# Kernel tuning notes

Measured on AMD Instinct MI355X. Metric: run time of the kernel, lower is better.

Reference implementation:

```python
import jax, jax.numpy as jnp
import numpy as np

B = 512; S = 6; Q = 2            # meta-batch, n_way*k_shot, n_way*q_query
DIM = 64; IMG = 28; N_WAY = 2
HEADS = 4; HD = DIM // HEADS     # retrieval heads / head dim
EPS = 1e-5


def _pool_mat(inp, out):
    # exact torch AdaptiveAvgPool2d windowing as a matrix [out, inp]
    P = np.zeros((out, inp), np.float32)
    for i in range(out):
        s = (i * inp) // out
        e = -((-(i + 1) * inp) // out)
        P[i, s:e] = 1.0 / (e - s)
    return jnp.asarray(P)

P28 = _pool_mat(IMG, 8)  # 28 -> 8; subsequent 8 -> 8 pools are identity


def _gelu(x):
    return jax.nn.gelu(x, approximate=False)


def _conv(x, w, b):
    y = jax.lax.conv_general_dilated(x, w, (1, 1), ((1, 1), (1, 1)),
                                     dimension_numbers=('NCHW', 'OIHW', 'NCHW'))
    return y + b[None, :, None, None]


def _bn(x, p):
    # p rows: gamma, beta, running_mean, running_var (eval-mode BatchNorm2d)
    g, bt, m, v = p[0], p[1], p[2], p[3]
    sc = g / jnp.sqrt(v + EPS)
    return (x - m[None, :, None, None]) * sc[None, :, None, None] + bt[None, :, None, None]


def _img_in(x, c1w, c1b, bn1, c2w, c2b, bn2, c3w, c3b, bn3, c4w, c4b, bn4, lin_w):
    h = _bn(_conv(x, c1w, c1b), bn1)
    h = jnp.einsum('oi,ncij,pj->ncop', P28, h, P28)   # adaptive avg pool 28x28 -> 8x8
    h = _gelu(h)                                       # dropout is identity in eval
    h = _gelu(_bn(_conv(h, c2w, c2b), bn2))
    h = _gelu(_bn(_conv(h, c3w, c3b), bn3))
    h = _gelu(_bn(_conv(h, c4w, c4b), bn4))            # -> [N,1,8,8]
    h = h.reshape(h.shape[0], -1)                      # [N,64]
    return h @ lin_w.T                                 # Linear(64 -> DIM, no bias)


def _net(x, w1, w2):
    # x: [B,K,D]; w1,w2: [B,D,D] batched fast weights
    h = jnp.einsum('bed,bkd->bke', w1, x)
    ah = _gelu(h)
    y = jnp.einsum('bed,bkd->bke', w2, ah)
    return y, h


def _get_lor(x, w1, w2, r_q, r_k, r_v, r_o, ln_w, ln_b):
    b, k, _ = x.shape
    q, _ = _net(x, w1, w2)
    qh = jnp.einsum('nhd,bkd->bknh', r_q, q)
    sc = jnp.einsum('bknh,rnh->bknr', qh, r_k) / (HD ** 0.5)
    p = jax.nn.softmax(sc, axis=-1)
    lor = jnp.einsum('bknr,rnh->bknh', p, r_v).reshape(b, k, DIM)
    lor = jnp.einsum('de,bkd->bke', r_o, lor)
    z = lor + x
    mu = z.mean(-1, keepdims=True)
    var = ((z - mu) ** 2).mean(-1, keepdims=True)
    return (z - mu) / jnp.sqrt(var + EPS) * ln_w + ln_b


def _forward(query_w, sxs, qxs, inner_lr, c1w, c1b, bn1, c2w, c2b, bn2, c3w, c3b, bn3,
             c4w, c4b, bn4, lin_w, emb, w1, w2, tags, r_q, r_k, r_v, r_o, ln_w, ln_b,
             sys, qys):
    b = query_w.shape[0]
    s = sxs.shape[1]
    q = qxs.shape[1]
    feats = lambda im: _img_in(im.reshape(-1, 1, IMG, IMG), c1w, c1b, bn1, c2w, c2b,
                               bn2, c3w, c3b, bn3, c4w, c4b, bn4, lin_w)
    sx = feats(sxs).reshape(b, s, DIM)
    qx = feats(qxs).reshape(b, q, DIM)
    qe = tags[4]
    w1b = jnp.broadcast_to(w1, (b, DIM, DIM))
    w2b = jnp.broadcast_to(w2, (b, DIM, DIM))
    bound = sx + emb[sys]                                          # [B,S,D]
    # all 4 tag variants for all S shots in one vectorized get_lor call
    inp = (bound[:, :, None, :] + tags[:4][None, None]).reshape(b, s * 4, DIM)
    lors = _get_lor(inp, w1b, w2b, r_q, r_k, r_v, r_o, ln_w, ln_b).reshape(b, s, 4, DIM)
    l1s, r1s, l2s, r2s = lors[:, :, 0], lors[:, :, 1], lors[:, :, 2], lors[:, :, 3]
    qw1 = w1[None] + jnp.einsum('bsl,bsr->blr', l1s, r1s)
    qw2 = w2[None] + jnp.einsum('bsl,bsr->blr', l2s, r2s)
    preds, _ = _net(qx + qe, qw1, qw2)                             # [B,Q,D]
    logits = jnp.einsum('ld,bqd->bql', emb, preds).reshape(-1, N_WAY)
    labels = qys.reshape(-1)
    ls = jax.nn.log_softmax(logits)
    task_loss = -jnp.take_along_axis(ls, labels[:, None], axis=1).mean()
    n_correct = (jnp.argmax(logits, axis=1) == labels).sum()
    return task_loss, n_correct, b * q


def setup_inputs() -> dict:
    key = jax.random.key(0)
    ks = jax.random.split(key, 24)
    rn = lambda i, sh, sc=1.0: sc * jax.random.normal(ks[i], sh, jnp.float32)
    def bnp(i, c):
        k0, k1, k2 = jax.random.split(ks[i], 3)
        return jnp.stack([1.0 + 0.1 * jax.random.normal(k0, (c,)),
                          0.1 * jax.random.normal(k1, (c,)),
                          0.1 * jax.random.normal(k2, (c,)),
                          0.5 + jax.random.uniform(jax.random.fold_in(ks[i], 3), (c,))])
    return {
        'query_w': rn(0, (B, DIM)),
        'sxs': rn(1, (B, S, IMG * IMG)),
        'qxs': rn(2, (B, Q, IMG * IMG)),
        'inner_lr': jnp.float32(0.1),
        'c1w': rn(3, (32, 1, 3, 3), 0.3), 'c1b': rn(4, (32,), 0.1), 'bn1': bnp(5, 32),
        'c2w': rn(6, (32, 32, 3, 3), 0.06), 'c2b': rn(7, (32,), 0.1), 'bn2': bnp(8, 32),
        'c3w': rn(9, (32, 32, 3, 3), 0.06), 'c3b': rn(10, (32,), 0.1), 'bn3': bnp(11, 32),
        'c4w': rn(12, (1, 32, 3, 3), 0.06), 'c4b': rn(13, (1,), 0.1), 'bn4': bnp(14, 1),
        'lin_w': rn(15, (DIM, 64), 0.125),
        'emb': rn(16, (N_WAY, DIM), 0.125),
        'w1': rn(17, (DIM, DIM), 0.125),
        'w2': rn(18, (DIM, DIM), 0.125),
        'tags': rn(19, (8, DIM), 0.125),
        'r_q': rn(20, (HEADS, HD, DIM), 0.125),
        'r_k': rn(21, (16, HEADS, HD), 0.25),
        'r_v': rn(22, (16, HEADS, HD), 0.25),
        'r_o': rn(23, (DIM, DIM), 0.125),
        'ln_w': 0.001 * jnp.ones((DIM,), jnp.float32),
        'ln_b': jnp.zeros((DIM,), jnp.float32),
        'sys': jax.random.randint(jax.random.fold_in(key, 100), (B, S), 0, N_WAY),
        'qys': jax.random.randint(jax.random.fold_in(key, 101), (B, Q), 0, N_WAY),
    }


def reference(query_w, sxs, qxs, inner_lr, c1w, c1b, bn1, c2w, c2b, bn2, c3w, c3b, bn3,
              c4w, c4b, bn4, lin_w, emb, w1, w2, tags, r_q, r_k, r_v, r_o, ln_w, ln_b,
              sys, qys):
    task_loss, n_correct, n_q = _forward(query_w, sxs, qxs, inner_lr, c1w, c1b, bn1,
                                         c2w, c2b, bn2, c3w, c3b, bn3, c4w, c4b, bn4,
                                         lin_w, emb, w1, w2, tags, r_q, r_k, r_v, r_o,
                                         ln_w, ln_b, sys, qys)
    return (task_loss, task_loss, jnp.float32(0.0), n_correct, n_q)
```

## Files before the change

kernel.cpp:

```cpp
#include <hip/hip_runtime.h>
#include <math.h>

constexpr int NSUP = 3072;
constexpr float EPSF = 1e-5f;

constexpr int WS_W1B  = 0;
constexpr int WS_B1   = 1024;
constexpr int WS_W2B  = 1056;
constexpr int WS_W3B  = 5664;
constexpr int WS_W4B  = 10272;
constexpr int WS_B4   = 10416;
constexpr int WS_B2   = 10420;
constexpr int WS_B3   = 10452;
constexpr int WS_HW1  = 10484;
constexpr int WS_HW2  = 12788;
constexpr int WS_HRQ  = 15092;
constexpr int WS_HROT = 17396;
constexpr int WS_PART = 19700;
constexpr int WS_FEATS= 20724;

using short8 = __attribute__((ext_vector_type(8))) short;
using f32x4  = __attribute__((ext_vector_type(4))) float;

__device__ __forceinline__ float gelu_f(float x) {
    return 0.5f * x * (1.0f + erff(x * 0.70710678118654752440f));
}
__device__ __forceinline__ unsigned short f2bf(float f) {
    unsigned u = __float_as_uint(f);
    return (unsigned short)((u + 0x7FFFu + ((u >> 16) & 1u)) >> 16);
}
__device__ __forceinline__ float bflo(unsigned u) { return __uint_as_float(u << 16); }
__device__ __forceinline__ float bfhi(unsigned u) { return __uint_as_float(u & 0xffff0000u); }

__global__ void __launch_bounds__(256) precompute_kernel(
    const float* __restrict__ c1w, const float* __restrict__ c1b, const float* __restrict__ bn1,
    const float* __restrict__ c2w, const float* __restrict__ c2b, const float* __restrict__ bn2,
    const float* __restrict__ c3w, const float* __restrict__ c3b, const float* __restrict__ bn3,
    const float* __restrict__ c4w, const float* __restrict__ c4b, const float* __restrict__ bn4,
    const float* __restrict__ w1, const float* __restrict__ w2,
    const float* __restrict__ rq, const float* __restrict__ ro,
    float* __restrict__ ws)
{
    const int gid = blockIdx.x * 256 + threadIdx.x;
    const int gsz = gridDim.x * 256;

    unsigned short* w1b = (unsigned short*)(ws + WS_W1B);
    for (int v = gid; v < 2048; v += gsz) {
        int kt = v >> 10, rem = v & 1023, oc = rem >> 5, kk = rem & 31;
        int tap = kt * 32 + kk;
        unsigned short o = 0;
        if (tap < 36) {
            int tt = tap / 6, s = tap - tt * 6;
            float sum = 0.f;
            for (int di = 0; di < 3; ++di) {
                int a = tt - di; if (a < 0 || a > 3) continue;
                for (int dj = 0; dj < 3; ++dj) {
                    int bb = s - dj; if (bb < 0 || bb > 3) continue;
                    sum += c1w[oc * 9 + di * 3 + dj];
                }
            }
            float sc1 = bn1[oc] * rsqrtf(bn1[96 + oc] + EPSF);
            o = f2bf(sum * sc1 * (1.0f / 16.0f));
        }
        w1b[v] = o;
    }
    for (int c = gid; c < 32; c += gsz) {
        float sc1 = bn1[c] * rsqrtf(bn1[96 + c] + EPSF);
        ws[WS_B1 + c] = (c1b[c] - bn1[64 + c]) * sc1 + bn1[32 + c];
        float sc2 = bn2[c] * rsqrtf(bn2[96 + c] + EPSF);
        ws[WS_B2 + c] = (c2b[c] - bn2[64 + c]) * sc2 + bn2[32 + c];
        float sc3 = bn3[c] * rsqrtf(bn3[96 + c] + EPSF);
        ws[WS_B3 + c] = (c3b[c] - bn3[64 + c]) * sc3 + bn3[32 + c];
    }
    unsigned short* w2b = (unsigned short*)(ws + WS_W2B);
    unsigned short* w3b = (unsigned short*)(ws + WS_W3B);
    for (int v = gid; v < 9216; v += gsz) {
        int tap = v >> 10, oc = (v >> 5) & 31, ic = v & 31;
        float sc2 = bn2[oc] * rsqrtf(bn2[96 + oc] + EPSF);
        float sc3 = bn3[oc] * rsqrtf(bn3[96 + oc] + EPSF);
        w2b[v] = f2bf(c2w[oc * 288 + ic * 9 + tap] * sc2);
        w3b[v] = f2bf(c3w[oc * 288 + ic * 9 + tap] * sc3);
    }
    {
        unsigned short* w4b = (unsigned short*)(ws + WS_W4B);
        float sc4 = bn4[0] * rsqrtf(bn4[3] + EPSF);
        for (int v = gid; v < 288; v += gsz) {
            int tap = v >> 5, ic = v & 31;
            w4b[v] = f2bf(c4w[ic * 9 + tap] * sc4);
        }
        if (gid == 0) ws[WS_B4] = (c4b[0] - bn4[2]) * sc4 + bn4[1];
    }
    unsigned short* hw1 = (unsigned short*)(ws + WS_HW1);
    unsigned short* hw2 = (unsigned short*)(ws + WS_HW2);
    unsigned short* hrq = (unsigned short*)(ws + WS_HRQ);
    unsigned short* hro = (unsigned short*)(ws + WS_HROT);
    for (int v = gid; v < 4608; v += gsz) {
        int e = v / 72, d = v - e * 72;
        unsigned short a = 0, b = 0, c = 0, r = 0;
        if (d < 64) {
            a = f2bf(w1[e * 64 + d]);
            b = f2bf(w2[e * 64 + d]);
            c = f2bf(rq[e * 64 + d]);
            r = f2bf(ro[d * 64 + e]);
        }
        hw1[v] = a; hw2[v] = b; hrq[v] = c; hro[v] = r;
    }
}

__global__ void __launch_bounds__(256, 4) feats_kernel(
    const float* __restrict__ sxs, const float* __restrict__ qxs,
    const float* __restrict__ lin_w, const float* __restrict__ ws,
    float* __restrict__ feats)
{
    __shared__ __align__(16) unsigned short sAct[4][3200];
    __shared__ __align__(16) float sh4[4][64];

    const int t    = threadIdx.x;
    const int wv   = t >> 6;
    const int lane = t & 63;
    const int col  = lane & 15;
    const int quad = lane >> 4;
    const int n    = blockIdx.x * 4 + wv;

    unsigned short* A = sAct[wv];

    {
        uint4 z = {0, 0, 0, 0};
        for (int i = lane; i < 400; i += 64) ((uint4*)A)[i] = z;
    }

    {
        const unsigned short* w1b = (const unsigned short*)(ws + WS_W1B);
        const float* img = (n < NSUP) ? (sxs + (size_t)n * 784) : (qxs + (size_t)(n - NSUP) * 784);
        int ttj[8], ssj[8];
        #pragma unroll
        for (int j = 0; j < 8; ++j) {
            int k = quad * 8 + j;
            ttj[j] = k / 6; ssj[j] = k - ttj[j] * 6;
        }
        f32x4 acc[4][2];
        #pragma unroll
        for (int mt = 0; mt < 4; ++mt) { acc[mt][0] = (f32x4){0,0,0,0}; acc[mt][1] = (f32x4){0,0,0,0}; }

        short8 b00 = *(const short8*)(w1b + (0 * 16 + col) * 32 + quad * 8);
        short8 b01 = *(const short8*)(w1b + (1 * 16 + col) * 32 + quad * 8);
        short8 b10 = *(const short8*)(w1b + 1024 + (0 * 16 + col) * 32 + quad * 8);
        short8 b11 = *(const short8*)(w1b + 1024 + (1 * 16 + col) * 32 + quad * 8);

        #pragma unroll
        for (int mt = 0; mt < 4; ++mt) {
            int px = mt * 16 + col;
            int sr = (((px >> 3) * 7) >> 1) - 1;
            int sc = (((px & 7) * 7) >> 1) - 1;
            short8 a0;
            #pragma unroll
            for (int j = 0; j < 8; ++j) {
                int rr = sr + ttj[j], cc = sc + ssj[j];
                float v = ((unsigned)rr < 28u && (unsigned)cc < 28u) ? img[rr * 28 + cc] : 0.f;
                a0[j] = (short)f2bf(v);
            }
            acc[mt][0] = __builtin_amdgcn_mfma_f32_16x16x32_bf16(a0, b00, acc[mt][0], 0, 0, 0);
            acc[mt][1] = __builtin_amdgcn_mfma_f32_16x16x32_bf16(a0, b01, acc[mt][1], 0, 0, 0);
            short8 a1 = {0,0,0,0,0,0,0,0};
            if (quad == 0) {
                #pragma unroll
                for (int j = 0; j < 4; ++j) {
                    int rr = sr + 5, cc = sc + 2 + j;
                    float v = ((unsigned)rr < 28u && (unsigned)cc < 28u) ? img[rr * 28 + cc] : 0.f;
                    a1[j] = (short)f2bf(v);
                }
            }
            acc[mt][0] = __builtin_amdgcn_mfma_f32_16x16x32_bf16(a1, b10, acc[mt][0], 0, 0, 0);
            acc[mt][1] = __builtin_amdgcn_mfma_f32_16x16x32_bf16(a1, b11, acc[mt][1], 0, 0, 0);
        }
        float bi0 = ws[WS_B1 + col], bi1 = ws[WS_B1 + 16 + col];
        #pragma unroll
        for (int mt = 0; mt < 4; ++mt)
            #pragma unroll
            for (int reg = 0; reg < 4; ++reg) {
                int px = mt * 16 + quad * 4 + reg;
                unsigned short* dst = A + (((px >> 3) + 1) * 10 + (px & 7) + 1) * 32;
                dst[col]      = f2bf(gelu_f(acc[mt][0][reg] + bi0));
                dst[col + 16] = f2bf(gelu_f(acc[mt][1][reg] + bi1));
            }
    }

    #pragma unroll 1
    for (int layer = 0; layer < 2; ++layer) {
        const unsigned short* wb = (const unsigned short*)(ws + (layer ? WS_W3B : WS_W2B));
        f32x4 acc[4][2];
        #pragma unroll
        for (int mt = 0; mt < 4; ++mt) { acc[mt][0] = (f32x4){0,0,0,0}; acc[mt][1] = (f32x4){0,0,0,0}; }
        const unsigned short* abase[4];
        #pragma unroll
        for (int mt = 0; mt < 4; ++mt) {
            int px = mt * 16 + col;
            abase[mt] = A + ((px >> 3) * 10 + (px & 7)) * 32 + quad * 8;
        }
        #pragma unroll
        for (int dr = 0; dr < 3; ++dr)
            #pragma unroll
            for (int dc = 0; dc < 3; ++dc) {
                int tap = dr * 3 + dc;
                short8 b0 = *(const short8*)(wb + (tap * 32 + col) * 32 + quad * 8);
                short8 b1 = *(const short8*)(wb + (tap * 32 + 16 + col) * 32 + quad * 8);
                #pragma unroll
                for (int mt = 0; mt < 4; ++mt) {
                    short8 a = *(const short8*)(abase[mt] + (dr * 10 + dc) * 32);
                    acc[mt][0] = __builtin_amdgcn_mfma_f32_16x16x32_bf16(a, b0, acc[mt][0], 0, 0, 0);
                    acc[mt][1] = __builtin_amdgcn_mfma_f32_16x16x32_bf16(a, b1, acc[mt][1], 0, 0, 0);
                }
            }
        float bi0 = ws[(layer ? WS_B3 : WS_B2) + col];
        float bi1 = ws[(layer ? WS_B3 : WS_B2) + 16 + col];
        #pragma unroll
        for (int mt = 0; mt < 4; ++mt)
            #pragma unroll
            for (int reg = 0; reg < 4; ++reg) {
                int px = mt * 16 + quad * 4 + reg;
                unsigned short* dst = A + (((px >> 3) + 1) * 10 + (px & 7) + 1) * 32;
                dst[col]      = f2bf(gelu_f(acc[mt][0][reg] + bi0));
                dst[col + 16] = f2bf(gelu_f(acc[mt][1][reg] + bi1));
            }
    }

    {
        f32x4 acc4[4];
        #pragma unroll
        for (int mt = 0; mt < 4; ++mt) acc4[mt] = (f32x4){0,0,0,0};
        const unsigned short* abase[4];
        #pragma unroll
        for (int mt = 0; mt < 4; ++mt) {
            int px = mt * 16 + col;
            abase[mt] = A + ((px >> 3) * 10 + (px & 7)) * 32 + quad * 8;
        }
        const unsigned short* w4g = (const unsigned short*)(ws + WS_W4B);
        #pragma unroll
        for (int dr = 0; dr < 3; ++dr)
            #pragma unroll
            for (int dc = 0; dc < 3; ++dc) {
                int tap = dr * 3 + dc;
                short8 b = *(const short8*)(w4g + tap * 32 + quad * 8);
                #pragma unroll
                for (int mt = 0; mt < 4; ++mt) {
                    short8 a = *(const short8*)(abase[mt] + (dr * 10 + dc) * 32);
                    acc4[mt] = __builtin_amdgcn_mfma_f32_16x16x32_bf16(a, b, acc4[mt], 0, 0, 0);
                }
            }
        if (col < 4) {
            f32x4 v = acc4[0];
            if (col == 1) v = acc4[1];
            else if (col == 2) v = acc4[2];
            else if (col == 3) v = acc4[3];
            float b4 = ws[WS_B4];
            #pragma unroll
            for (int reg = 0; reg < 4; ++reg)
                sh4[wv][col * 16 + quad * 4 + reg] = gelu_f(v[reg] + b4);
        }
    }

    {
        const float4* lw = (const float4*)(lin_w + (size_t)lane * 64);
        const float4* hp = (const float4*)sh4[wv];
        float acc = 0.f;
        #pragma unroll
        for (int j = 0; j < 16; ++j) {
            float4 w = lw[j], h = hp[j];
            acc += w.x * h.x + w.y * h.y + w.z * h.z + w.w * h.w;
        }
        feats[n * 64 + lane] = acc;
    }
}

__device__ __forceinline__ void head_gemm(const unsigned short* __restrict__ Ab,
                                          const unsigned short* __restrict__ Bw,
                                          int col, int quad, int wvid, f32x4 res[2])
{
    #pragma unroll
    for (int u = 0; u < 2; ++u) {
        int tau = wvid + u * 4;
        int mt = tau & 1, nt = tau >> 1;
        f32x4 acc = {0, 0, 0, 0};
        #pragma unroll
        for (int kt = 0; kt < 2; ++kt) {
            short8 a = *(const short8*)(Ab + (mt * 16 + col) * 72 + kt * 32 + quad * 8);
            short8 b = *(const short8*)(Bw + (nt * 16 + col) * 72 + kt * 32 + quad * 8);
            acc = __builtin_amdgcn_mfma_f32_16x16x32_bf16(a, b, acc, 0, 0, 0);
        }
        res[u] = acc;
    }
}

__global__ void __launch_bounds__(256, 4) head_kernel(
    const float* __restrict__ emb, const float* __restrict__ tags,
    const float* __restrict__ rk, const float* __restrict__ rv,
    const float* __restrict__ lnw, const float* __restrict__ lnb,
    const int* __restrict__ sys, const int* __restrict__ qys,
    const float* __restrict__ ws, const float* __restrict__ feats,
    float* __restrict__ part)
{
    __shared__ __align__(16) unsigned short bufA[2304], bufB[2304];
    __shared__ __align__(16) float sXf[1536];
    __shared__ __align__(16) float s_xq[128], s_ah[128], s_yp[128];
    __shared__ float s_t1[12], s_t2[12], s_mu[24], s_rs[24], s_lg[4];

    const int t    = threadIdx.x;
    const int b    = blockIdx.x;
    const int wvid = t >> 6;
    const int col  = t & 15;
    const int quad = (t >> 4) & 3;

    const unsigned short* W1g = (const unsigned short*)(ws + WS_HW1);
    const unsigned short* W2g = (const unsigned short*)(ws + WS_HW2);
    const unsigned short* RQg = (const unsigned short*)(ws + WS_HRQ);
    const unsigned short* ROg = (const unsigned short*)(ws + WS_HROT);

    if (t < 72) {
        uint4 z = {0, 0, 0, 0};
        ((uint4*)(bufA + 1728))[t] = z;
        ((uint4*)(bufB + 1728))[t] = z;
    }
    for (int idx = t; idx < 1536; idx += 256) {
        int k = idx >> 6, e = idx & 63;
        int s = k >> 2, tg = k & 3;
        int cls = sys[b * 6 + s];
        float v = feats[(b * 6 + s) * 64 + e] + emb[cls * 64 + e] + tags[tg * 64 + e];
        sXf[idx] = v;
        bufA[k * 72 + e] = f2bf(v);
    }
    __syncthreads();

    f32x4 r[2];
    head_gemm(bufA, W1g, col, quad, wvid, r);
    #pragma unroll
    for (int u = 0; u < 2; ++u) {
        int tau = wvid + u * 4, mt = tau & 1, nt = tau >> 1;
        #pragma unroll
        for (int reg = 0; reg < 4; ++reg) {
            int row = mt * 16 + quad * 4 + reg;
            if (row < 24) bufB[row * 72 + nt * 16 + col] = f2bf(gelu_f(r[u][reg]));
        }
    }
    __syncthreads();
    head_gemm(bufB, W2g, col, quad, wvid, r);
    #pragma unroll
    for (int u = 0; u < 2; ++u) {
        int tau = wvid + u * 4, mt = tau & 1, nt = tau >> 1;
        #pragma unroll
        for (int reg = 0; reg < 4; ++reg) {
            int row = mt * 16 + quad * 4 + reg;
            if (row < 24) bufA[row * 72 + nt * 16 + col] = f2bf(r[u][reg]);
        }
    }
    __syncthreads();
    head_gemm(bufA, RQg, col, quad, wvid, r);
    #pragma unroll
    for (int u = 0; u < 2; ++u) {
        int tau = wvid + u * 4, mt = tau & 1, nt = tau >> 1;
        #pragma unroll
        for (int reg = 0; reg < 4; ++reg) {
            int row = mt * 16 + quad * 4 + reg;
            if (row < 24) bufB[row * 72 + nt * 16 + col] = f2bf(r[u][reg]);
        }
    }
    __syncthreads();

    if (t < 96) {
        int k = t >> 2, nn = t & 3;
        const unsigned short* qp = bufB + k * 72 + nn * 16;
        uint4 u0 = *(const uint4*)(qp);
        uint4 u1 = *(const uint4*)(qp + 8);
        float qv[16];
        qv[0]=bflo(u0.x); qv[1]=bfhi(u0.x); qv[2]=bflo(u0.y); qv[3]=bfhi(u0.y);
        qv[4]=bflo(u0.z); qv[5]=bfhi(u0.z); qv[6]=bflo(u0.w); qv[7]=bfhi(u0.w);
        qv[8]=bflo(u1.x); qv[9]=bfhi(u1.x); qv[10]=bflo(u1.y); qv[11]=bfhi(u1.y);
        qv[12]=bflo(u1.z); qv[13]=bfhi(u1.z); qv[14]=bflo(u1.w); qv[15]=bfhi(u1.w);
        float sc[16]; float mx = -1e30f;
        #pragma unroll
        for (int rr = 0; rr < 16; ++rr) {
            const float* kp = rk + rr * 64 + nn * 16;
            float d = 0.f;
            #pragma unroll
            for (int h = 0; h < 16; ++h) d += qv[h] * kp[h];
            d *= 0.25f;
            sc[rr] = d; mx = fmaxf(mx, d);
        }
        float sum = 0.f;
        #pragma unroll
        for (int rr = 0; rr < 16; ++rr) { sc[rr] = expf(sc[rr] - mx); sum += sc[rr]; }
        float inv = 1.0f / sum;
        float o[16];
        #pragma unroll
        for (int h = 0; h < 16; ++h) o[h] = 0.f;
        #pragma unroll
        for (int rr = 0; rr < 16; ++rr) {
            const float* vp = rv + rr * 64 + nn * 16;
            float p = sc[rr];
            #pragma unroll
            for (int h = 0; h < 16; ++h) o[h] += p * vp[h];
        }
        unsigned short* op = bufA + k * 72 + nn * 16;
        #pragma unroll
        for (int h = 0; h < 16; ++h) op[h] = f2bf(o[h] * inv);
    }
    __syncthreads();

    head_gemm(bufA, ROg, col, quad, wvid, r);
    #pragma unroll
    for (int u = 0; u < 2; ++u) {
        int tau = wvid + u * 4, mt = tau & 1, nt = tau >> 1;
        #pragma unroll
        for (int reg = 0; reg < 4; ++reg) {
            int row = mt * 16 + quad * 4 + reg;
            if (row < 24) {
                int idx = row * 64 + nt * 16 + col;
                sXf[idx] = sXf[idx] + r[u][reg];
            }
        }
    }
    __syncthreads();

    if (t < 24) {
        const float4* zp = (const float4*)(sXf + t * 64);
        float sx_ = 0.f;
        #pragma unroll
        for (int j = 0; j < 16; ++j) {
            float4 v = zp[(j + t) & 15];
            sx_ += v.x + v.y + v.z + v.w;
        }
        float mu = sx_ * (1.0f / 64.0f);
        float vv = 0.f;
        #pragma unroll
        for (int j = 0; j < 16; ++j) {
            float4 v = zp[(j + t) & 15];
            float d0 = v.x - mu, d1 = v.y - mu, d2 = v.z - mu, d3 = v.w - mu;
            vv += d0*d0 + d1*d1 + d2*d2 + d3*d3;
        }
        s_mu[t] = mu;
        s_rs[t] = 1.0f / sqrtf(vv * (1.0f / 64.0f) + EPSF);
    }
    __syncthreads();
    for (int idx = t; idx < 1536; idx += 256) {
        int k = idx >> 6, e = idx & 63;
        float v = (sXf[idx] - s_mu[k]) * s_rs[k] * lnw[e] + lnb[e];
        bufB[k * 72 + e] = f2bf(v);
    }
    if (t < 128) {
        int q = t >> 6, e = t & 63;
        s_xq[t] = feats[(NSUP + b * 2 + q) * 64 + e] + tags[256 + e];
    }
    __syncthreads();

    if (t < 12) {
        int q = t / 6, s = t - q * 6;
        const uint4* rp = (const uint4*)(bufB + (s * 4 + 1) * 72);
        const float* xp = s_xq + q * 64;
        float d = 0.f;
        #pragma unroll
        for (int j = 0; j < 8; ++j) {
            uint4 u = rp[j];
            const float* x = xp + j * 8;
            d += bflo(u.x)*x[0] + bfhi(u.x)*x[1] + bflo(u.y)*x[2] + bfhi(u.y)*x[3]
               + bflo(u.z)*x[4] + bfhi(u.z)*x[5] + bflo(u.w)*x[6] + bfhi(u.w)*x[7];
        }
        s_t1[t] = d;
    }
    __syncthreads();
    if (t < 128) {
        int q = t >> 6, e = t & 63;
        const uint4* wp = (const uint4*)(W1g + e * 72);
        const float* xp = s_xq + q * 64;
        float acc = 0.f;
        #pragma unroll
        for (int j = 0; j < 8; ++j) {
            uint4 u = wp[j];
            const float* x = xp + j * 8;
            acc += bflo(u.x)*x[0] + bfhi(u.x)*x[1] + bflo(u.y)*x[2] + bfhi(u.y)*x[3]
                 + bflo(u.z)*x[4] + bfhi(u.z)*x[5] + bflo(u.w)*x[6] + bfhi(u.w)*x[7];
        }
        #pragma unroll
        for (int s = 0; s < 6; ++s)
            acc += bflo((unsigned)bufB[(s * 4 + 0) * 72 + e]) * s_t1[q * 6 + s];
        s_ah[t] = gelu_f(acc);
    }
    __syncthreads();
    if (t < 12) {
        int q = t / 6, s = t - q * 6;
        const uint4* rp = (const uint4*)(bufB + (s * 4 + 3) * 72);
        const float* xp = s_ah + q * 64;
        float d = 0.f;
        #pragma unroll
        for (int j = 0; j < 8; ++j) {
            uint4 u = rp[j];
            const float* x = xp + j * 8;
            d += bflo(u.x)*x[0] + bfhi(u.x)*x[1] + bflo(u.y)*x[2] + bfhi(u.y)*x[3]
               + bflo(u.z)*x[4] + bfhi(u.z)*x[5] + bflo(u.w)*x[6] + bfhi(u.w)*x[7];
        }
        s_t2[t] = d;
    }
    __syncthreads();
    if (t < 128) {
        int q = t >> 6, e = t & 63;
        const uint4* wp = (const uint4*)(W2g + e * 72);
        const float* xp = s_ah + q * 64;
        float acc = 0.f;
        #pragma unroll
        for (int j = 0; j < 8; ++j) {
            uint4 u = wp[j];
            const float* x = xp + j * 8;
            acc += bflo(u.x)*x[0] + bfhi(u.x)*x[1] + bflo(u.y)*x[2] + bfhi(u.y)*x[3]
                 + bflo(u.z)*x[4] + bfhi(u.z)*x[5] + bflo(u.w)*x[6] + bfhi(u.w)*x[7];
        }
        #pragma unroll
        for (int s = 0; s < 6; ++s)
            acc += bflo((unsigned)bufB[(s * 4 + 2) * 72 + e]) * s_t2[q * 6 + s];
        s_yp[t] = acc;
    }
    __syncthreads();
    if (t < 4) {
        int q = t >> 1, ll = t & 1;
        const float4* ep = (const float4*)(emb + ll * 64);
        const float4* yp = (const float4*)(s_yp + q * 64);
        float d = 0.f;
        #pragma unroll
        for (int j = 0; j < 16; ++j) {
            float4 a = ep[j], x = yp[j];
            d += a.x*x.x + a.y*x.y + a.z*x.z + a.w*x.w;
        }
        s_lg[t] = d;
    }
    __syncthreads();
    if (t == 0) {
        float lsum = 0.f, corr = 0.f;
        #pragma unroll
        for (int q = 0; q < 2; ++q) {
            float l0 = s_lg[q * 2], l1 = s_lg[q * 2 + 1];
            int lab = qys[b * 2 + q];
            float m = fmaxf(l0, l1);
            float lse = m + logf(expf(l0 - m) + expf(l1 - m));
            lsum += -((lab ? l1 : l0) - lse);
            int pred = (l1 > l0) ? 1 : 0;
            corr += (pred == lab) ? 1.0f : 0.0f;
        }
        part[b] = lsum;
        part[512 + b] = corr;
    }
}

__global__ void __launch_bounds__(256) finalize_kernel(const float* __restrict__ part,
                                                       float* __restrict__ out)
{
    __shared__ float sl[256], sc[256];
    const int t = threadIdx.x;
    sl[t] = part[t] + part[t + 256];
    sc[t] = part[512 + t] + part[768 + t];
    __syncthreads();
    for (int s = 128; s > 0; s >>= 1) {
        if (t < s) { sl[t] += sl[t + s]; sc[t] += sc[t + s]; }
        __syncthreads();
    }
    if (t == 0) {
        float loss = sl[0] * (1.0f / 1024.0f);
        out[0] = loss;
        out[1] = loss;
        out[2] = 0.0f;
        out[3] = sc[0];
        out[4] = 1024.0f;
    }
}

extern "C" void kernel_launch(void* const* d_in, const int* in_sizes, int n_in,
                              void* d_out, int out_size, void* d_ws, size_t ws_size,
                              hipStream_t stream)
{
    (void)in_sizes; (void)n_in; (void)out_size; (void)ws_size;
    const float* sxs  = (const float*)d_in[1];
    const float* qxs  = (const float*)d_in[2];
    const float* c1w  = (const float*)d_in[4];
    const float* c1b  = (const float*)d_in[5];
    const float* bn1  = (const float*)d_in[6];
    const float* c2w  = (const float*)d_in[7];
    const float* c2b  = (const float*)d_in[8];
    const float* bn2  = (const float*)d_in[9];
    const float* c3w  = (const float*)d_in[10];
    const float* c3b  = (const float*)d_in[11];
    const float* bn3  = (const float*)d_in[12];
    const float* c4w  = (const float*)d_in[13];
    const float* c4b  = (const float*)d_in[14];
    const float* bn4  = (const float*)d_in[15];
    const float* lin_w= (const float*)d_in[16];
    const float* emb  = (const float*)d_in[17];
    const float* w1   = (const float*)d_in[18];
    const float* w2   = (const float*)d_in[19];
    const float* tags = (const float*)d_in[20];
    const float* rq   = (const float*)d_in[21];
    const float* rk   = (const float*)d_in[22];
    const float* rv   = (const float*)d_in[23];
    const float* ro   = (const float*)d_in[24];
    const float* lnw  = (const float*)d_in[25];
    const float* lnb  = (const float*)d_in[26];
    const int*   sys  = (const int*)d_in[27];
    const int*   qys  = (const int*)d_in[28];

    float* ws  = (float*)d_ws;
    float* out = (float*)d_out;

    precompute_kernel<<<64, 256, 0, stream>>>(c1w, c1b, bn1, c2w, c2b, bn2,
                                              c3w, c3b, bn3, c4w, c4b, bn4,
                                              w1, w2, rq, ro, ws);
    feats_kernel<<<1024, 256, 0, stream>>>(sxs, qxs, lin_w, ws, ws + WS_FEATS);
    head_kernel<<<512, 256, 0, stream>>>(emb, tags, rk, rv, lnw, lnb, sys, qys,
                                         ws, ws + WS_FEATS, ws + WS_PART);
    finalize_kernel<<<1, 256, 0, stream>>>(ws + WS_PART, out);
}
```

Baseline: 175.7 us.

## Fuse feature extraction and per-task head into one 512-thread kernel

```diff
diff --git a/kernel.cpp b/kernel.cpp
--- a/kernel.cpp
+++ b/kernel.cpp
@@ -1,7 +1,6 @@
 #include <hip/hip_runtime.h>
 #include <math.h>
 
-constexpr int NSUP = 3072;
 constexpr float EPSF = 1e-5f;
 
 constexpr int WS_W1B  = 0;
@@ -17,7 +16,6 @@
 constexpr int WS_HRQ  = 15092;
 constexpr int WS_HROT = 17396;
 constexpr int WS_PART = 19700;
-constexpr int WS_FEATS= 20724;
 
 using short8 = __attribute__((ext_vector_type(8))) short;
 using f32x4  = __attribute__((ext_vector_type(4))) float;
@@ -107,23 +105,51 @@
     }
 }
 
-__global__ void __launch_bounds__(256, 4) feats_kernel(
+__device__ __forceinline__ f32x4 head_gemm8(const unsigned short* __restrict__ Ab,
+                                            const unsigned short* __restrict__ Bw,
+                                            int col, int quad, int tau)
+{
+    int mt = tau & 1, nt = tau >> 1;
+    f32x4 acc = {0, 0, 0, 0};
+    #pragma unroll
+    for (int kt = 0; kt < 2; ++kt) {
+        short8 a = *(const short8*)(Ab + (mt * 16 + col) * 72 + kt * 32 + quad * 8);
+        short8 b = *(const short8*)(Bw + (nt * 16 + col) * 72 + kt * 32 + quad * 8);
+        acc = __builtin_amdgcn_mfma_f32_16x16x32_bf16(a, b, acc, 0, 0, 0);
+    }
+    return acc;
+}
+
+__global__ void __launch_bounds__(512, 2) fused_kernel(
     const float* __restrict__ sxs, const float* __restrict__ qxs,
-    const float* __restrict__ lin_w, const float* __restrict__ ws,
-    float* __restrict__ feats)
+    const float* __restrict__ lin_w,
+    const float* __restrict__ emb, const float* __restrict__ tags,
+    const float* __restrict__ rk, const float* __restrict__ rv,
+    const float* __restrict__ lnw, const float* __restrict__ lnb,
+    const int* __restrict__ sys, const int* __restrict__ qys,
+    const float* __restrict__ ws, float* __restrict__ part)
 {
-    __shared__ __align__(16) unsigned short sAct[4][3200];
-    __shared__ __align__(16) float sh4[4][64];
+    __shared__ __align__(16) unsigned short sAct[8][3200];
+    __shared__ __align__(16) float sFeat[8][64];
+    __shared__ __align__(16) unsigned short bufA[2304], bufB[2304];
+    __shared__ __align__(16) float sXf[1536];
+    __shared__ __align__(16) float s_xq[128], s_ah[128], s_yp[128];
+    __shared__ float s_t1[12], s_t2[12], s_mu[24], s_rs[24], s_lg[4];
 
     const int t    = threadIdx.x;
+    const int b    = blockIdx.x;
     const int wv   = t >> 6;
     const int lane = t & 63;
     const int col  = lane & 15;
     const int quad = lane >> 4;
-    const int n    = blockIdx.x * 4 + wv;
 
     unsigned short* A = sAct[wv];
 
+    if (t < 72) {
+        uint4 z = {0, 0, 0, 0};
+        ((uint4*)(bufA + 1728))[t] = z;
+        ((uint4*)(bufB + 1728))[t] = z;
+    }
     {
         uint4 z = {0, 0, 0, 0};
         for (int i = lane; i < 400; i += 64) ((uint4*)A)[i] = z;
@@ -131,7 +157,8 @@
 
     {
         const unsigned short* w1b = (const unsigned short*)(ws + WS_W1B);
-        const float* img = (n < NSUP) ? (sxs + (size_t)n * 784) : (qxs + (size_t)(n - NSUP) * 784);
+        const float* img = (wv < 6) ? (sxs + ((size_t)b * 6 + wv) * 784)
+                                    : (qxs + ((size_t)b * 2 + (wv - 6)) * 784);
         int ttj[8], ssj[8];
         #pragma unroll
         for (int j = 0; j < 8; ++j) {
@@ -240,11 +267,11 @@
             #pragma unroll
             for (int dc = 0; dc < 3; ++dc) {
                 int tap = dr * 3 + dc;
-                short8 b = *(const short8*)(w4g + tap * 32 + quad * 8);
+                short8 bb = *(const short8*)(w4g + tap * 32 + quad * 8);
                 #pragma unroll
                 for (int mt = 0; mt < 4; ++mt) {
                     short8 a = *(const short8*)(abase[mt] + (dr * 10 + dc) * 32);
-                    acc4[mt] = __builtin_amdgcn_mfma_f32_16x16x32_bf16(a, b, acc4[mt], 0, 0, 0);
+                    acc4[mt] = __builtin_amdgcn_mfma_f32_16x16x32_bf16(a, bb, acc4[mt], 0, 0, 0);
                 }
             }
         if (col < 4) {
@@ -255,112 +282,74 @@
             float b4 = ws[WS_B4];
             #pragma unroll
             for (int reg = 0; reg < 4; ++reg)
-                sh4[wv][col * 16 + quad * 4 + reg] = gelu_f(v[reg] + b4);
-        }
-    }
-
-    {
+                A[3000 + col * 16 + quad * 4 + reg] = 0;
+            #pragma unroll
+            for (int reg = 0; reg < 4; ++reg)
+                sFeat[wv][col * 16 + quad * 4 + reg] = gelu_f(v[reg] + b4);
+        }
+    }
+    {
+        float h4[64];
+        const float4* hp = (const float4*)sFeat[wv];
+        #pragma unroll
+        for (int j = 0; j < 16; ++j) *(float4*)&h4[j * 4] = hp[j];
         const float4* lw = (const float4*)(lin_w + (size_t)lane * 64);
-        const float4* hp = (const float4*)sh4[wv];
         float acc = 0.f;
         #pragma unroll
         for (int j = 0; j < 16; ++j) {
-            float4 w = lw[j], h = hp[j];
-            acc += w.x * h.x + w.y * h.y + w.z * h.z + w.w * h.w;
-        }
-        feats[n * 64 + lane] = acc;
-    }
-}
-
-__device__ __forceinline__ void head_gemm(const unsigned short* __restrict__ Ab,
-                                          const unsigned short* __restrict__ Bw,
-                                          int col, int quad, int wvid, f32x4 res[2])
-{
-    #pragma unroll
-    for (int u = 0; u < 2; ++u) {
-        int tau = wvid + u * 4;
-        int mt = tau & 1, nt = tau >> 1;
-        f32x4 acc = {0, 0, 0, 0};
-        #pragma unroll
-        for (int kt = 0; kt < 2; ++kt) {
-            short8 a = *(const short8*)(Ab + (mt * 16 + col) * 72 + kt * 32 + quad * 8);
-            short8 b = *(const short8*)(Bw + (nt * 16 + col) * 72 + kt * 32 + quad * 8);
-            acc = __builtin_amdgcn_mfma_f32_16x16x32_bf16(a, b, acc, 0, 0, 0);
-        }
-        res[u] = acc;
-    }
-}
-
-__global__ void __launch_bounds__(256, 4) head_kernel(
-    const float* __restrict__ emb, const float* __restrict__ tags,
-    const float* __restrict__ rk, const float* __restrict__ rv,
-    const float* __restrict__ lnw, const float* __restrict__ lnb,
-    const int* __restrict__ sys, const int* __restrict__ qys,
-    const float* __restrict__ ws, const float* __restrict__ feats,
-    float* __restrict__ part)
-{
-    __shared__ __align__(16) unsigned short bufA[2304], bufB[2304];
-    __shared__ __align__(16) float sXf[1536];
-    __shared__ __align__(16) float s_xq[128], s_ah[128], s_yp[128];
-    __shared__ float s_t1[12], s_t2[12], s_mu[24], s_rs[24], s_lg[4];
-
-    const int t    = threadIdx.x;
-    const int b    = blockIdx.x;
-    const int wvid = t >> 6;
-    const int col  = t & 15;
-    const int quad = (t >> 4) & 3;
+            float4 w = lw[j];
+            acc += w.x * h4[j*4] + w.y * h4[j*4+1] + w.z * h4[j*4+2] + w.w * h4[j*4+3];
+        }
+        sFeat[wv][lane] = acc;
+    }
+    __syncthreads();
+
+    for (int idx = t; idx < 1536; idx += 512) {
+        int k = idx >> 6, e = idx & 63;
+        int s = k >> 2, tg = k & 3;
+        int cls = sys[b * 6 + s];
+        float v = sFeat[s][e] + emb[cls * 64 + e] + tags[tg * 64 + e];
+        sXf[idx] = v;
+        bufA[k * 72 + e] = f2bf(v);
+    }
+    if (t < 128) {
+        int q = t >> 6, e = t & 63;
+        s_xq[t] = sFeat[6 + q][e] + tags[256 + e];
+    }
+    __syncthreads();
 
     const unsigned short* W1g = (const unsigned short*)(ws + WS_HW1);
     const unsigned short* W2g = (const unsigned short*)(ws + WS_HW2);
     const unsigned short* RQg = (const unsigned short*)(ws + WS_HRQ);
     const unsigned short* ROg = (const unsigned short*)(ws + WS_HROT);
 
-    if (t < 72) {
-        uint4 z = {0, 0, 0, 0};
-        ((uint4*)(bufA + 1728))[t] = z;
-        ((uint4*)(bufB + 1728))[t] = z;
-    }
-    for (int idx = t; idx < 1536; idx += 256) {
-        int k = idx >> 6, e = idx & 63;
-        int s = k >> 2, tg = k & 3;
-        int cls = sys[b * 6 + s];
-        float v = feats[(b * 6 + s) * 64 + e] + emb[cls * 64 + e] + tags[tg * 64 + e];
-        sXf[idx] = v;
-        bufA[k * 72 + e] = f2bf(v);
-    }
-    __syncthreads();
-
-    f32x4 r[2];
-    head_gemm(bufA, W1g, col, quad, wvid, r);
-    #pragma unroll
-    for (int u = 0; u < 2; ++u) {
-        int tau = wvid + u * 4, mt = tau & 1, nt = tau >> 1;
+    {
+        f32x4 r = head_gemm8(bufA, W1g, col, quad, wv);
+        int mt = wv & 1, nt = wv >> 1;
         #pragma unroll
         for (int reg = 0; reg < 4; ++reg) {
             int row = mt * 16 + quad * 4 + reg;
-            if (row < 24) bufB[row * 72 + nt * 16 + col] = f2bf(gelu_f(r[u][reg]));
-        }
-    }
-    __syncthreads();
-    head_gemm(bufB, W2g, col, quad, wvid, r);
-    #pragma unroll
-    for (int u = 0; u < 2; ++u) {
-        int tau = wvid + u * 4, mt = tau & 1, nt = tau >> 1;
+            if (row < 24) bufB[row * 72 + nt * 16 + col] = f2bf(gelu_f(r[reg]));
+        }
+    }
+    __syncthreads();
+    {
+        f32x4 r = head_gemm8(bufB, W2g, col, quad, wv);
+        int mt = wv & 1, nt = wv >> 1;
         #pragma unroll
         for (int reg = 0; reg < 4; ++reg) {
             int row = mt * 16 + quad * 4 + reg;
-            if (row < 24) bufA[row * 72 + nt * 16 + col] = f2bf(r[u][reg]);
-        }
-    }
-    __syncthreads();
-    head_gemm(bufA, RQg, col, quad, wvid, r);
-    #pragma unroll
-    for (int u = 0; u < 2; ++u) {
-        int tau = wvid + u * 4, mt = tau & 1, nt = tau >> 1;
+            if (row < 24) bufA[row * 72 + nt * 16 + col] = f2bf(r[reg]);
+        }
+    }
+    __syncthreads();
+    {
+        f32x4 r = head_gemm8(bufA, RQg, col, quad, wv);
+        int mt = wv & 1, nt = wv >> 1;
         #pragma unroll
         for (int reg = 0; reg < 4; ++reg) {
             int row = mt * 16 + quad * 4 + reg;
-            if (row < 24) bufB[row * 72 + nt * 16 + col] = f2bf(r[u][reg]);
+            if (row < 24) bufB[row * 72 + nt * 16 + col] = f2bf(r[reg]);
         }
     }
     __syncthreads();
@@ -405,16 +394,15 @@
     }
     __syncthreads();
 
-    head_gemm(bufA, ROg, col, quad, wvid, r);
-    #pragma unroll
-    for (int u = 0; u < 2; ++u) {
-        int tau = wvid + u * 4, mt = tau & 1, nt = tau >> 1;
+    {
+        f32x4 r = head_gemm8(bufA, ROg, col, quad, wv);
+        int mt = wv & 1, nt = wv >> 1;
         #pragma unroll
         for (int reg = 0; reg < 4; ++reg) {
             int row = mt * 16 + quad * 4 + reg;
             if (row < 24) {
                 int idx = row * 64 + nt * 16 + col;
-                sXf[idx] = sXf[idx] + r[u][reg];
+                sXf[idx] = sXf[idx] + r[reg];
             }
         }
     }
@@ -440,14 +428,10 @@
         s_rs[t] = 1.0f / sqrtf(vv * (1.0f / 64.0f) + EPSF);
     }
     __syncthreads();
-    for (int idx = t; idx < 1536; idx += 256) {
+    for (int idx = t; idx < 1536; idx += 512) {
         int k = idx >> 6, e = idx & 63;
         float v = (sXf[idx] - s_mu[k]) * s_rs[k] * lnw[e] + lnb[e];
         bufB[k * 72 + e] = f2bf(v);
-    }
-    if (t < 128) {
-        int q = t >> 6, e = t & 63;
-        s_xq[t] = feats[(NSUP + b * 2 + q) * 64 + e] + tags[256 + e];
     }
     __syncthreads();
 
@@ -608,8 +592,7 @@
     precompute_kernel<<<64, 256, 0, stream>>>(c1w, c1b, bn1, c2w, c2b, bn2,
                                               c3w, c3b, bn3, c4w, c4b, bn4,
                                               w1, w2, rq, ro, ws);
-    feats_kernel<<<1024, 256, 0, stream>>>(sxs, qxs, lin_w, ws, ws + WS_FEATS);
-    head_kernel<<<512, 256, 0, stream>>>(emb, tags, rk, rv, lnw, lnb, sys, qys,
-                                         ws, ws + WS_FEATS, ws + WS_PART);
+    fused_kernel<<<512, 512, 0, stream>>>(sxs, qxs, lin_w, emb, tags, rk, rv,
+                                          lnw, lnb, sys, qys, ws, ws + WS_PART);
     finalize_kernel<<<1, 256, 0, stream>>>(ws + WS_PART, out);
 }
```

Result: slower. 192.5 us (+9.5%).
